# Optimization experiments

Hardware: AMD Instinct MI355X
Metric: run time of the kernel (lower is better)

Reference implementation:

```python
import jax, jax.numpy as jnp
import numpy as np

D_MODEL = 512
NUM_HEADS = 8
DFF = 2048
EPS = 1e-5


def _layernorm(x, gamma, beta):
    mu = jnp.mean(x, axis=-1, keepdims=True)
    var = jnp.mean(jnp.square(x - mu), axis=-1, keepdims=True)
    return (x - mu) / jnp.sqrt(var + EPS) * gamma + beta


def _mha(xq, xkv, wq, bq, wk, bk, wv, bv, wo, bo, mask):
    B, Sq, D = xq.shape
    Sk = xkv.shape[1]
    H = NUM_HEADS
    depth = D // H
    q = (xq @ wq + bq).reshape(B, Sq, H, depth).transpose(0, 2, 1, 3)  # bhqd
    k = (xkv @ wk + bk).reshape(B, Sk, H, depth).transpose(0, 2, 1, 3)  # bhkd
    v = (xkv @ wv + bv).reshape(B, Sk, H, depth).transpose(0, 2, 1, 3)  # bhkd
    logits = jnp.einsum('bhqd,bhkd->bhqk', q, k) / jnp.sqrt(jnp.float32(depth))
    if mask is not None:
        logits = logits + mask * -10000.0
    attn = jax.nn.softmax(logits, axis=-1)  # [B,H,Sq,Sk]
    out = jnp.einsum('bhqk,bhkd->bhqd', attn, v)
    out = out.transpose(0, 2, 1, 3).reshape(B, Sq, D)
    return out @ wo + bo, attn


def setup_inputs() -> dict:
    key = jax.random.key(0)
    ks = jax.random.split(key, 32)
    B, T, S, D, F = 8, 1024, 1024, D_MODEL, DFF
    sd = 1.0 / np.sqrt(D)
    inp = {
        'x': jax.random.normal(ks[0], (B, T, D), jnp.float32),
        'enc_output': jax.random.normal(ks[1], (B, S, D), jnp.float32),
        # causal mask: 1 where attention is disallowed (future positions)
        'look_ahead_mask': (1.0 - jnp.tril(jnp.ones((T, T), jnp.float32)))[None, None],
        'padding_mask': jnp.zeros((1, 1, 1, S), jnp.float32),
    }
    i = 2
    for pfx in ('1', '2'):
        for nm in ('wq', 'wk', 'wv', 'wo'):
            inp[nm + pfx] = jax.random.normal(ks[i], (D, D), jnp.float32) * sd; i += 1
            inp['b' + nm[1] + pfx if False else nm.replace('w', 'b') + pfx] = jnp.zeros((D,), jnp.float32)
    inp['w_ff1'] = jax.random.normal(ks[i], (D, F), jnp.float32) * sd; i += 1
    inp['b_ff1'] = jnp.zeros((F,), jnp.float32)
    inp['w_ff2'] = jax.random.normal(ks[i], (F, D), jnp.float32) / np.sqrt(F); i += 1
    inp['b_ff2'] = jnp.zeros((D,), jnp.float32)
    for j in ('1', '2', '3'):
        inp['gamma' + j] = jnp.ones((D,), jnp.float32)
        inp['beta' + j] = jnp.zeros((D,), jnp.float32)
    return inp


def reference(x, enc_output, look_ahead_mask, padding_mask,
              wq1, bq1, wk1, bk1, wv1, bv1, wo1, bo1,
              wq2, bq2, wk2, bk2, wv2, bv2, wo2, bo2,
              w_ff1, b_ff1, w_ff2, b_ff2,
              gamma1, beta1, gamma2, beta2, gamma3, beta3):
    # self-attention (dropout is identity: training=False)
    sa, sa_w = _mha(x, x, wq1, bq1, wk1, bk1, wv1, bv1, wo1, bo1, look_ahead_mask)
    out1 = _layernorm(x + sa, gamma1, beta1)
    # cross-attention
    ca, ca_w = _mha(out1, enc_output, wq2, bq2, wk2, bk2, wv2, bv2, wo2, bo2, padding_mask)
    out2 = _layernorm(out1 + ca, gamma2, beta2)
    # FFN
    ff = jax.nn.relu(out2 @ w_ff1 + b_ff1) @ w_ff2 + b_ff2
    out3 = _layernorm(out2 + ff, gamma3, beta3)
    return out3, sa_w, ca_w
```

## Files before the change

### kernel.cpp

```cpp
#include <hip/hip_runtime.h>
#include <hip/hip_bf16.h>


using bf16 = __hip_bfloat16;
typedef __attribute__((ext_vector_type(8))) short bf16x8v;
typedef __attribute__((ext_vector_type(4))) float f32x4;
typedef __attribute__((ext_vector_type(2))) float f32x2;
typedef __attribute__((ext_vector_type(2))) unsigned int u32x2;

#define DEVI __device__ __forceinline__

#define QSCL 0.18033688011112042f

DEVI short f2bs(float f) {
  bf16 h = __float2bfloat16(f);
  return *reinterpret_cast<short*>(&h);
}
DEVI bf16 f2b(float f) { return __float2bfloat16(f); }
DEVI float ex2(float x) { return __builtin_amdgcn_exp2f(x); }
DEVI float ldf(const float* p) { return *p; }
DEVI float ldf(const bf16* p) { return __bfloat162float(*p); }

DEVI void gload16(const bf16* g, bf16* l) {
  __builtin_amdgcn_global_load_lds(
      (const __attribute__((address_space(1))) void*)g,
      (__attribute__((address_space(3))) void*)l, 16, 0, 0);
}

DEVI void vmwait(int n) {
  if (n == 0)       asm volatile("s_waitcnt vmcnt(0)" ::: "memory");
  else if (n == 1)  asm volatile("s_waitcnt vmcnt(1)" ::: "memory");
  else if (n == 2)  asm volatile("s_waitcnt vmcnt(2)" ::: "memory");
  else if (n == 4)  asm volatile("s_waitcnt vmcnt(4)" ::: "memory");
  else if (n == 6)  asm volatile("s_waitcnt vmcnt(6)" ::: "memory");
  else if (n == 8)  asm volatile("s_waitcnt vmcnt(8)" ::: "memory");
  else              asm volatile("s_waitcnt vmcnt(10)" ::: "memory");
}
#define SBAR() __builtin_amdgcn_sched_barrier(0)

struct WDesc { const float* src; bf16* dst; int K; int N; int toff; float scl; };
struct PrepPack {
  const float* x; const float* enc; bf16* xb; bf16* encb;
  WDesc d[10];
  const float* bsrc[6]; float bscl[6]; float* bdst;
};

__global__ __launch_bounds__(256) void prep_k(PrepPack p) {
  const int bid = blockIdx.x;
  if (bid < 8192) {
    const float* s = (bid < 4096) ? p.x : p.enc;
    bf16* d = (bid < 4096) ? p.xb : p.encb;
    long i = ((long)(bid & 4095) * 256 + threadIdx.x) * 4;
    f32x4 v = *reinterpret_cast<const f32x4*>(s + i);
    union { short sh[4]; long l; } u;
    u.sh[0] = f2bs(v[0]); u.sh[1] = f2bs(v[1]); u.sh[2] = f2bs(v[2]); u.sh[3] = f2bs(v[3]);
    *reinterpret_cast<long*>(d + i) = u.l;
    return;
  }
  if (bid < 12288) {
    const int t = bid - 8192;
    int wi = 0;
#pragma unroll
    for (int i = 1; i < 10; i++)
      if (t >= p.d[i].toff) wi = i;
    const WDesc d = p.d[wi];
    const int lt = t - d.toff;
    const int nx = d.N >> 5;
    const int n0 = (lt % nx) * 32, k0 = (lt / nx) * 32;
    __shared__ float tile[32][33];
    const int tx = threadIdx.x & 31, ty = threadIdx.x >> 5;
#pragma unroll
    for (int i = 0; i < 32; i += 8)
      tile[ty + i][tx] = d.src[(long)(k0 + ty + i) * d.N + n0 + tx] * d.scl;
    __syncthreads();
#pragma unroll
    for (int i = 0; i < 32; i += 8)
      d.dst[(long)(n0 + ty + i) * d.K + k0 + tx] = f2b(tile[tx][ty + i]);
    return;
  }
  const int i = bid - 12288;
  const int e = threadIdx.x * 2;
  f32x2 v = *reinterpret_cast<const f32x2*>(p.bsrc[i] + e);
  v[0] *= p.bscl[i]; v[1] *= p.bscl[i];
  *reinterpret_cast<f32x2*>(p.bdst + i * 512 + e) = v;
}

template <int FM, int FN, typename TC, bool RELU, bool VTOUT>
DEVI void gemm_body(int bid, int nblocks,
                    const bf16* __restrict__ A, int lda,
                    const bf16* __restrict__ Bt, int ldb,
                    TC* __restrict__ C, int ldc,
                    const float* __restrict__ bias, int K, int tiles_n,
                    bf16* sA, bf16* sB,
                    bf16* __restrict__ vtout, int vcol0) {
  constexpr int BM = 32 * FM, BN = 32 * FN;
  const int tm8 = (nblocks / tiles_n) >> 3;
  const int r8 = bid >> 3;
  const int tm = (bid & 7) + ((r8 % tm8) << 3);
  const int tn = r8 / tm8;
  const int tid = threadIdx.x, wave = tid >> 6, lane = tid & 63;
  const int wr = wave >> 1, wc = wave & 1;
  const int l16 = lane & 15, lhi = lane >> 4;
  const int srow = lane >> 2, scol = (lane & 3) * 8;

  const bf16* Ab = A + (long)(tm * BM + wave * (BM / 4) + srow) * lda + scol;
  const bf16* Bb = Bt + (long)(tn * BN + wave * (BN / 4) + srow) * ldb + scol;

  auto stage = [&](int buf, int k0) {
#pragma unroll
    for (int i = 0; i < BM / 64; i++)
      gload16(Ab + (long)(i * 16) * lda + k0, sA + buf * BM * 32 + (wave * (BM / 4) + i * 16) * 32);
#pragma unroll
    for (int i = 0; i < BN / 64; i++)
      gload16(Bb + (long)(i * 16) * ldb + k0, sB + buf * BN * 32 + (wave * (BN / 4) + i * 16) * 32);
  };

  stage(0, 0);
  __syncthreads();

  f32x4 acc[FM][FN] = {};
  int cur = 0;
  for (int k0 = 0; k0 < K; k0 += 32) {
    if (k0 + 32 < K) stage(cur ^ 1, k0 + 32);
    bf16x8v af[FM], bfr[FN];
#pragma unroll
    for (int m = 0; m < FM; m++)
      af[m] = *reinterpret_cast<const bf16x8v*>(
          sA + cur * BM * 32 + (wr * 16 * FM + m * 16 + l16) * 32 + lhi * 8);
#pragma unroll
    for (int n = 0; n < FN; n++)
      bfr[n] = *reinterpret_cast<const bf16x8v*>(
          sB + cur * BN * 32 + (wc * 16 * FN + n * 16 + l16) * 32 + lhi * 8);
#pragma unroll
    for (int m = 0; m < FM; m++)
#pragma unroll
      for (int n = 0; n < FN; n++)
        acc[m][n] = __builtin_amdgcn_mfma_f32_16x16x32_bf16(af[m], bfr[n], acc[m][n], 0, 0, 0);
    if (k0 + 32 < K) {
      __syncthreads();
      cur ^= 1;
    }
  }

#pragma unroll
  for (int m = 0; m < FM; m++) {
    const int gr0 = tm * BM + wr * 16 * FM + m * 16 + lhi * 4;
#pragma unroll
    for (int n = 0; n < FN; n++) {
      const int gc = tn * BN + wc * 16 * FN + n * 16 + l16;
      const float bv = bias ? bias[gc] : 0.f;
      if (VTOUT && gc >= vcol0) {
        const int vc = gc - vcol0;
        bf16* vdst = vtout + ((long)(((gr0 >> 10) << 3) + (vc >> 6)) << 16)
                           + ((long)(vc & 63) << 10) + (gr0 & 1023);
        union { short sh[4]; u32x2 u2; } pk;
#pragma unroll
        for (int j = 0; j < 4; j++) pk.sh[j] = f2bs(acc[m][n][j] + bv);
        *reinterpret_cast<u32x2*>(vdst) = pk.u2;
      } else {
#pragma unroll
        for (int j = 0; j < 4; j++) {
          float v = acc[m][n][j] + bv;
          if (RELU) v = fmaxf(v, 0.f);
          if constexpr (sizeof(TC) == 4)
            C[(long)(gr0 + j) * ldc + gc] = v;
          else
            C[(long)(gr0 + j) * ldc + gc] = f2b(v);
        }
      }
    }
  }
}

template <int FM, int FN, typename TC, bool RELU>
__global__ __launch_bounds__(256) void gemm_gl_k(
    const bf16* __restrict__ A, int lda, const bf16* __restrict__ Bt, int ldb,
    TC* __restrict__ C, int ldc, const float* __restrict__ bias, int K, int tiles_n) {
  __shared__ bf16 sA[2 * 32 * FM * 32];
  __shared__ bf16 sB[2 * 32 * FN * 32];
  gemm_body<FM, FN, TC, RELU, false>(blockIdx.x, gridDim.x, A, lda, Bt, ldb, C, ldc,
                                     bias, K, tiles_n, sA, sB, nullptr, 0);
}

__global__ __launch_bounds__(256) void gemm_qkv_k(
    const bf16* __restrict__ A, const bf16* __restrict__ Bt, bf16* __restrict__ C,
    const float* __restrict__ bias, bf16* __restrict__ vt) {
  __shared__ bf16 sA[2 * 128 * 32];
  __shared__ bf16 sB[2 * 128 * 32];
  gemm_body<4, 4, bf16, false, true>(blockIdx.x, gridDim.x, A, 512, Bt, 512, C, 1536,
                                     bias, 512, 12, sA, sB, vt, 1024);
}

template <bool CAUSAL>
DEVI void attn_body(int bid, char* smem,
                    const bf16* __restrict__ Qm, int ldq,
                    const bf16* __restrict__ Km, int ldk,
                    const bf16* __restrict__ vt,
                    float* __restrict__ P, bf16* __restrict__ ctx) {
  bf16* Kst = (bf16*)smem;
  bf16* Vst = Kst + 3 * 2048;
  bf16* pst = Vst + 3 * 2048;
  const int bh = bid & 63;
  const int g = bid >> 6;
  const int qx = CAUSAL ? ((g < 4) ? g : 11 - g) : g;
  const int b = bh >> 3, h = bh & 7;
  const int tid = threadIdx.x, wave = tid >> 6, lane = tid & 63;
  const int l16 = lane & 15, lhi = lane >> 4;
  const int q0 = qx * 128 + wave * 32;
  const bf16* Qb = Qm + (long)(b * 1024 + q0) * ldq + h * 64;
  const bf16* Kb = Km + (long)b * 1024 * ldk + h * 64;
  const bf16* Vb = vt + (long)bh * 64 * 1024;

  const int nun = CAUSAL ? (q0 >> 5) : 32;
  const int nchw = CAUSAL ? nun + 1 : 32;
  const int nchb = CAUSAL ? qx * 4 + 4 : 32;

  const bf16* ksrc = Kb + (long)(tid >> 3) * ldk + ((tid & 7) ^ ((tid >> 3) & 7)) * 8;
  const bf16* vsrc = Vb + (long)(tid >> 2) * 1024 + ((tid & 3) ^ ((tid >> 2) & 3)) * 8;

  int kfo[2][2];
#pragma unroll
  for (int cc = 0; cc < 2; cc++) {
    const int r = cc * 16 + l16;
#pragma unroll
    for (int ks = 0; ks < 2; ks++)
      kfo[cc][ks] = r * 64 + (((ks * 64 + lhi * 16) ^ ((r & 7) << 4)) >> 1);
  }
  int vfo[4];
#pragma unroll
  for (int n = 0; n < 4; n++) {
    const int r = n * 16 + l16;
    vfo[n] = r * 32 + (((lhi * 16) ^ ((r & 3) << 4)) >> 1);
  }

  bf16x8v qB[2][2];
#pragma unroll
  for (int m = 0; m < 2; m++)
#pragma unroll
    for (int ks = 0; ks < 2; ks++)
      qB[m][ks] = *reinterpret_cast<const bf16x8v*>(
          Qb + (long)(m * 16 + l16) * ldq + ks * 32 + lhi * 8);

  float ll[2] = {0.f, 0.f};

  gload16(ksrc, Kst + wave * 512);
  gload16(ksrc + (long)32 * ldk, Kst + 2048 + wave * 512);
#pragma unroll 1
  for (int ch = 0; ch < nchb; ch++) {
    if (ch + 1 < nchb) vmwait(1); else vmwait(0);
    SBAR();
    __builtin_amdgcn_s_barrier();
    SBAR();
    if (ch + 2 < nchb)
      gload16(ksrc + (long)(ch + 2) * 32 * ldk, Kst + ((ch + 2) % 3) * 2048 + wave * 512);
    if (ch < nchw) {
      const int bo = (ch % 3) * 2048;
      bf16x8v kf[2][2];
#pragma unroll
      for (int cc = 0; cc < 2; cc++)
#pragma unroll
        for (int ks = 0; ks < 2; ks++)
          kf[cc][ks] = *reinterpret_cast<const bf16x8v*>(&Kst[bo + kfo[cc][ks]]);
      const bool diag = CAUSAL && (ch == nun);
#pragma unroll
      for (int m = 0; m < 2; m++) {
        f32x4 s0 = {}, s1 = {};
        s0 = __builtin_amdgcn_mfma_f32_16x16x32_bf16(kf[0][0], qB[m][0], s0, 0, 0, 0);
        s0 = __builtin_amdgcn_mfma_f32_16x16x32_bf16(kf[0][1], qB[m][1], s0, 0, 0, 0);
        s1 = __builtin_amdgcn_mfma_f32_16x16x32_bf16(kf[1][0], qB[m][0], s1, 0, 0, 0);
        s1 = __builtin_amdgcn_mfma_f32_16x16x32_bf16(kf[1][1], qB[m][1], s1, 0, 0, 0);
        if (diag) {
          const int rq = m * 16 + l16;
#pragma unroll
          for (int j = 0; j < 4; j++) {
            s0[j] = (lhi * 4 + j <= rq) ? s0[j] : -1e30f;
            s1[j] = (16 + lhi * 4 + j <= rq) ? s1[j] : -1e30f;
          }
        }
        float sum = 0.f;
#pragma unroll
        for (int j = 0; j < 4; j++) sum += ex2(s0[j]) + ex2(s1[j]);
        ll[m] += sum;
      }
    }
  }
  __syncthreads();

  float il[2];
#pragma unroll
  for (int m = 0; m < 2; m++) {
    float lo = ll[m];
    lo += __shfl_xor(lo, 16);
    lo += __shfl_xor(lo, 32);
    il[m] = 1.f / lo;
  }

  f32x4 pv[2][4] = {};
  float* Pg = P + (long)bh * 1024 * 1024 + (long)q0 * 1024;
  gload16(ksrc, Kst + wave * 512);
  gload16(vsrc, Vst + wave * 512);
  gload16(ksrc + (long)32 * ldk, Kst + 2048 + wave * 512);
  gload16(vsrc + 32, Vst + 2048 + wave * 512);
#pragma unroll 1
  for (int ch = 0; ch < nchb; ch++) {
    const int Sa = (ch >= 2 && ch - 2 < nchw) ? 4 : 0;
    const int Lr = (ch + 1 < nchb) ? 2 : 0;
    const int Sb = (ch >= 1 && ch - 1 < nchw) ? 4 : 0;
    vmwait(Sa + Lr + Sb);
    SBAR();
    __builtin_amdgcn_s_barrier();
    SBAR();
    if (ch + 2 < nchb) {
      gload16(ksrc + (long)(ch + 2) * 32 * ldk, Kst + ((ch + 2) % 3) * 2048 + wave * 512);
      gload16(vsrc + (ch + 2) * 32, Vst + ((ch + 2) % 3) * 2048 + wave * 512);
    }
    if (ch < nchw) {
      const int kc = ch * 32;
      const int bo = (ch % 3) * 2048;
      bf16x8v kf[2][2], vf[4];
#pragma unroll
      for (int cc = 0; cc < 2; cc++)
#pragma unroll
        for (int ks = 0; ks < 2; ks++)
          kf[cc][ks] = *reinterpret_cast<const bf16x8v*>(&Kst[bo + kfo[cc][ks]]);
#pragma unroll
      for (int n = 0; n < 4; n++)
        vf[n] = *reinterpret_cast<const bf16x8v*>(&Vst[bo + vfo[n]]);
      const bool diag = CAUSAL && (ch == nun);
#pragma unroll
      for (int m = 0; m < 2; m++) {
        f32x4 s0 = {}, s1 = {};
        s0 = __builtin_amdgcn_mfma_f32_16x16x32_bf16(kf[0][0], qB[m][0], s0, 0, 0, 0);
        s0 = __builtin_amdgcn_mfma_f32_16x16x32_bf16(kf[0][1], qB[m][1], s0, 0, 0, 0);
        s1 = __builtin_amdgcn_mfma_f32_16x16x32_bf16(kf[1][0], qB[m][0], s1, 0, 0, 0);
        s1 = __builtin_amdgcn_mfma_f32_16x16x32_bf16(kf[1][1], qB[m][1], s1, 0, 0, 0);
        if (diag) {
          const int rq = m * 16 + l16;
#pragma unroll
          for (int j = 0; j < 4; j++) {
            s0[j] = (lhi * 4 + j <= rq) ? s0[j] : -1e30f;
            s1[j] = (16 + lhi * 4 + j <= rq) ? s1[j] : -1e30f;
          }
        }
        f32x4 p0, p1;
#pragma unroll
        for (int j = 0; j < 4; j++) {
          p0[j] = ex2(s0[j]) * il[m];
          p1[j] = ex2(s1[j]) * il[m];
        }
        const int prow = (m * 16 + l16) * 40;
        union { short s[4]; u32x2 u; } pk0, pk1;
#pragma unroll
        for (int j = 0; j < 4; j++) { pk0.s[j] = f2bs(p0[j]); pk1.s[j] = f2bs(p1[j]); }
        *reinterpret_cast<u32x2*>(&pst[wave * 1280 + prow + lhi * 4]) = pk0.u;
        *reinterpret_cast<u32x2*>(&pst[wave * 1280 + prow + 16 + lhi * 4]) = pk1.u;
      }
#pragma unroll
      for (int m = 0; m < 2; m++) {
        bf16x8v pa = *reinterpret_cast<const bf16x8v*>(
            &pst[wave * 1280 + (m * 16 + l16) * 40 + lhi * 8]);
#pragma unroll
        for (int n = 0; n < 4; n++)
          pv[m][n] = __builtin_amdgcn_mfma_f32_16x16x32_bf16(pa, vf[n], pv[m][n], 0, 0, 0);
      }
#pragma unroll
      for (int f = 0; f < 4; f++) {
        const int row = f * 8 + (lane >> 3);
        u32x2 raw = *reinterpret_cast<const u32x2*>(
            &pst[wave * 1280 + row * 40 + (lane & 7) * 4]);
        union { unsigned int u; float fl; } c0, c1, c2, c3;
        c0.u = raw[0] << 16; c1.u = raw[0] & 0xffff0000u;
        c2.u = raw[1] << 16; c3.u = raw[1] & 0xffff0000u;
        f32x4 val = {c0.fl, c1.fl, c2.fl, c3.fl};
        __builtin_nontemporal_store(
            val, reinterpret_cast<f32x4*>(Pg + (long)row * 1024 + kc + (lane & 7) * 4));
      }
    }
  }

  bf16* cb = ctx + (long)(b * 1024 + q0) * 512 + h * 64;
#pragma unroll
  for (int m = 0; m < 2; m++)
#pragma unroll
    for (int n = 0; n < 4; n++)
#pragma unroll
      for (int j = 0; j < 4; j++)
        cb[(long)(m * 16 + lhi * 4 + j) * 512 + n * 16 + l16] = f2b(pv[m][n][j]);
}

template <bool CAUSAL>
__global__ __launch_bounds__(256) void attn_k(
    const bf16* __restrict__ Qm, int ldq, const bf16* __restrict__ Km, int ldk,
    const bf16* __restrict__ vt, float* __restrict__ P, bf16* __restrict__ ctx) {
  __shared__ __align__(16) char smem[34816];
  attn_body<CAUSAL>(blockIdx.x, smem, Qm, ldq, Km, ldk, vt, P, ctx);
}

__global__ __launch_bounds__(256) void attn_gemm_k(
    const bf16* __restrict__ Qm, int ldq, const bf16* __restrict__ Km, int ldk,
    const bf16* __restrict__ vt, float* __restrict__ P, bf16* __restrict__ ctx,
    const bf16* __restrict__ A, int lda, const bf16* __restrict__ Bt, int ldb,
    bf16* __restrict__ C, int ldc, const float* __restrict__ bias, int K, int tiles_n,
    bf16* __restrict__ vt2) {
  __shared__ __align__(16) char smem[34816];
  if (blockIdx.x < 512) {
    attn_body<true>(blockIdx.x, smem, Qm, ldq, Km, ldk, vt, P, ctx);
  } else {
    bf16* sA = (bf16*)smem;
    gemm_body<4, 4, bf16, false, true>(blockIdx.x - 512, 512, A, lda, Bt, ldb,
                                       C, ldc, bias, K, tiles_n, sA, sA + 8192,
                                       vt2, 512);
  }
}

template <typename TR>
__global__ __launch_bounds__(512) void gemm_ln_k(
    const bf16* __restrict__ A, int lda, const bf16* __restrict__ Bt,
    const float* __restrict__ bias, const TR* __restrict__ resid,
    const float* __restrict__ gamma, const float* __restrict__ beta,
    float* __restrict__ outf, bf16* __restrict__ outb, int K) {
  __shared__ bf16 sA[2][32 * 32];
  __shared__ bf16 sB[2][512 * 32];
  __shared__ float red[2][32][8];
  __shared__ f32x2 mr[32];
  const int tm = blockIdx.x;
  const int tid = threadIdx.x, wave = tid >> 6, lane = tid & 63;
  const int l16 = lane & 15, lhi = lane >> 4;

  const bf16* Asrc = A + (long)(tm * 32 + (tid >> 2)) * lda + (tid & 3) * 8;
  const bf16* Bsrc = Bt + (long)(tid >> 2) * K + (tid & 3) * 8;

  auto stage = [&](int buf, int k0) {
    if (tid < 128) gload16(Asrc + k0, &sA[buf][(tid >> 6) * 512]);
#pragma unroll
    for (int p = 0; p < 4; p++)
      gload16(Bsrc + (long)(p * 128) * K + k0, &sB[buf][p * 4096 + wave * 512]);
  };

  stage(0, 0);
  __syncthreads();

  f32x4 acc[2][4] = {};
  int cur = 0;
  for (int k0 = 0; k0 < K; k0 += 32) {
    if (k0 + 32 < K) stage(cur ^ 1, k0 + 32);
    bf16x8v af[2], bfr[4];
#pragma unroll
    for (int m = 0; m < 2; m++)
      af[m] = *reinterpret_cast<const bf16x8v*>(&sA[cur][(m * 16 + l16) * 32 + lhi * 8]);
#pragma unroll
    for (int n = 0; n < 4; n++)
      bfr[n] = *reinterpret_cast<const bf16x8v*>(&sB[cur][(wave * 64 + n * 16 + l16) * 32 + lhi * 8]);
#pragma unroll
    for (int m = 0; m < 2; m++)
#pragma unroll
      for (int n = 0; n < 4; n++)
        acc[m][n] = __builtin_amdgcn_mfma_f32_16x16x32_bf16(af[m], bfr[n], acc[m][n], 0, 0, 0);
    if (k0 + 32 < K) {
      __syncthreads();
      cur ^= 1;
    }
  }

  float bv[4], gm[4], bt[4];
#pragma unroll
  for (int n = 0; n < 4; n++) {
    const int gc = wave * 64 + n * 16 + l16;
    bv[n] = bias[gc]; gm[n] = gamma[gc]; bt[n] = beta[gc];
  }
  float v[2][4][4], rs[2][4], rq[2][4];
#pragma unroll
  for (int m = 0; m < 2; m++)
#pragma unroll
    for (int j = 0; j < 4; j++) { rs[m][j] = 0.f; rq[m][j] = 0.f; }
#pragma unroll
  for (int m = 0; m < 2; m++) {
#pragma unroll
    for (int j = 0; j < 4; j++) {
      const long grow = tm * 32 + m * 16 + lhi * 4 + j;
#pragma unroll
      for (int n = 0; n < 4; n++) {
        const int gc = wave * 64 + n * 16 + l16;
        const float val = acc[m][n][j] + bv[n] + ldf(resid + grow * 512 + gc);
        v[m][n][j] = val;
        rs[m][j] += val;
        rq[m][j] += val * val;
      }
    }
  }
#pragma unroll
  for (int m = 0; m < 2; m++)
#pragma unroll
    for (int j = 0; j < 4; j++)
#pragma unroll
      for (int off = 1; off <= 8; off <<= 1) {
        rs[m][j] += __shfl_xor(rs[m][j], off);
        rq[m][j] += __shfl_xor(rq[m][j], off);
      }
  if (l16 == 0) {
#pragma unroll
    for (int m = 0; m < 2; m++)
#pragma unroll
      for (int j = 0; j < 4; j++) {
        red[0][m * 16 + lhi * 4 + j][wave] = rs[m][j];
        red[1][m * 16 + lhi * 4 + j][wave] = rq[m][j];
      }
  }
  __syncthreads();
  if (tid < 32) {
    float s = 0.f, q = 0.f;
#pragma unroll
    for (int w = 0; w < 8; w++) { s += red[0][tid][w]; q += red[1][tid][w]; }
    const float mean = s * (1.f / 512.f);
    const float var = q * (1.f / 512.f) - mean * mean;
    f32x2 o = {mean, rsqrtf(var + 1e-5f)};
    mr[tid] = o;
  }
  __syncthreads();
#pragma unroll
  for (int m = 0; m < 2; m++) {
#pragma unroll
    for (int j = 0; j < 4; j++) {
      const int row = m * 16 + lhi * 4 + j;
      const f32x2 mrv = mr[row];
      const long grow = tm * 32 + row;
#pragma unroll
      for (int n = 0; n < 4; n++) {
        const int gc = wave * 64 + n * 16 + l16;
        const float o = (v[m][n][j] - mrv[0]) * mrv[1] * gm[n] + bt[n];
        if (outf) outf[grow * 512 + gc] = o;
        if (outb) outb[grow * 512 + gc] = f2b(o);
      }
    }
  }
}

extern "C" void kernel_launch(void* const* d_in, const int* in_sizes, int n_in,
                              void* d_out, int out_size, void* d_ws, size_t ws_size,
                              hipStream_t stream) {
  const float* x = (const float*)d_in[0];
  const float* enc = (const float*)d_in[1];
  const float* wq1 = (const float*)d_in[4];  const float* bq1 = (const float*)d_in[5];
  const float* wk1 = (const float*)d_in[6];  const float* bk1 = (const float*)d_in[7];
  const float* wv1 = (const float*)d_in[8];  const float* bv1 = (const float*)d_in[9];
  const float* wo1 = (const float*)d_in[10]; const float* bo1 = (const float*)d_in[11];
  const float* wq2 = (const float*)d_in[12]; const float* bq2 = (const float*)d_in[13];
  const float* wk2 = (const float*)d_in[14]; const float* bk2 = (const float*)d_in[15];
  const float* wv2 = (const float*)d_in[16]; const float* bv2 = (const float*)d_in[17];
  const float* wo2 = (const float*)d_in[18]; const float* bo2 = (const float*)d_in[19];
  const float* wff1 = (const float*)d_in[20]; const float* bff1 = (const float*)d_in[21];
  const float* wff2 = (const float*)d_in[22]; const float* bff2 = (const float*)d_in[23];
  const float* gamma1 = (const float*)d_in[24]; const float* beta1 = (const float*)d_in[25];
  const float* gamma2 = (const float*)d_in[26]; const float* beta2 = (const float*)d_in[27];
  const float* gamma3 = (const float*)d_in[28]; const float* beta3 = (const float*)d_in[29];

  float* out3 = (float*)d_out;
  float* sa_w = out3 + (long)8 * 1024 * 512;
  float* ca_w = sa_w + (long)64 * 1024 * 1024;

  char* w = (char*)d_ws;
  auto alloc = [&](long bytes) { char* p = w; w += (bytes + 255) & ~255L; return p; };
  bf16* xb     = (bf16*)alloc(8192L * 512 * 2);
  bf16* encb   = (bf16*)alloc(8192L * 512 * 2);
  bf16* wqkv1t = (bf16*)alloc(1536L * 512 * 2);
  bf16* wo1t   = (bf16*)alloc(512L * 512 * 2);
  bf16* wq2t   = (bf16*)alloc(512L * 512 * 2);
  bf16* wkv2t  = (bf16*)alloc(1024L * 512 * 2);
  bf16* wo2t   = (bf16*)alloc(512L * 512 * 2);
  bf16* wff1t  = (bf16*)alloc(2048L * 512 * 2);
  bf16* wff2t  = (bf16*)alloc(512L * 2048 * 2);
  float* bcat  = (float*)alloc(3072L * 4);
  bf16* qkv    = (bf16*)alloc(8192L * 1536 * 2);
  bf16* q2b    = (bf16*)alloc(8192L * 512 * 2);
  bf16* kv2    = (bf16*)alloc(8192L * 1024 * 2);
  bf16* vt     = (bf16*)alloc(64L * 64 * 1024 * 2);
  bf16* vt2    = (bf16*)alloc(64L * 64 * 1024 * 2);
  bf16* ctx    = (bf16*)alloc(8192L * 512 * 2);
  bf16* out1b  = (bf16*)alloc(8192L * 512 * 2);
  bf16* out2b  = (bf16*)alloc(8192L * 512 * 2);
  bf16* ffh    = qkv;

  PrepPack pp;
  pp.x = x; pp.enc = enc; pp.xb = xb; pp.encb = encb;
  pp.d[0] = {wq1,  wqkv1t,               512,  512,  0,    QSCL};
  pp.d[1] = {wk1,  wqkv1t + 512L * 512,  512,  512,  256,  1.f};
  pp.d[2] = {wv1,  wqkv1t + 1024L * 512, 512,  512,  512,  1.f};
  pp.d[3] = {wo1,  wo1t,                 512,  512,  768,  1.f};
  pp.d[4] = {wq2,  wq2t,                 512,  512,  1024, QSCL};
  pp.d[5] = {wk2,  wkv2t,                512,  512,  1280, 1.f};
  pp.d[6] = {wv2,  wkv2t + 512L * 512,   512,  512,  1536, 1.f};
  pp.d[7] = {wo2,  wo2t,                 512,  512,  1792, 1.f};
  pp.d[8] = {wff1, wff1t,                512,  2048, 2048, 1.f};
  pp.d[9] = {wff2, wff2t,                2048, 512,  3072, 1.f};
  pp.bsrc[0] = bq1; pp.bsrc[1] = bk1; pp.bsrc[2] = bv1;
  pp.bsrc[3] = bk2; pp.bsrc[4] = bv2; pp.bsrc[5] = bq2;
  pp.bscl[0] = QSCL; pp.bscl[1] = 1.f; pp.bscl[2] = 1.f;
  pp.bscl[3] = 1.f;  pp.bscl[4] = 1.f; pp.bscl[5] = QSCL;
  pp.bdst = bcat;
  prep_k<<<12294, 256, 0, stream>>>(pp);

  gemm_qkv_k<<<768, 256, 0, stream>>>(xb, wqkv1t, qkv, bcat, vt);
  attn_gemm_k<<<1024, 256, 0, stream>>>(
      qkv, 1536, qkv + 512, 1536, vt, sa_w, ctx,
      encb, 512, wkv2t, 512, kv2, 1024, bcat + 1536, 512, 8, vt2);
  gemm_ln_k<float><<<256, 512, 0, stream>>>(
      ctx, 512, wo1t, bo1, x, gamma1, beta1, nullptr, out1b, 512);

  gemm_gl_k<2, 4, bf16, false><<<512, 256, 0, stream>>>(
      out1b, 512, wq2t, 512, q2b, 512, bcat + 2560, 512, 4);
  attn_k<false><<<512, 256, 0, stream>>>(
      q2b, 512, kv2, 1024, vt2, ca_w, ctx);
  gemm_ln_k<bf16><<<256, 512, 0, stream>>>(
      ctx, 512, wo2t, bo2, out1b, gamma2, beta2, nullptr, out2b, 512);

  gemm_gl_k<4, 4, bf16, true><<<1024, 256, 0, stream>>>(
      out2b, 512, wff1t, 512, ffh, 2048, bff1, 512, 16);
  gemm_ln_k<bf16><<<256, 512, 0, stream>>>(
      ffh, 2048, wff2t, bff2, out2b, gamma3, beta3, out3, nullptr, 2048);
}
```

Measured before the change: 370.3 us.

## Replace QKV and FFN1 GEMMs with 256x256-tile 8-wave GEMM kernel

Adds a new GEMM kernel using 256x256 output tiles, a K-step of 64, 512 threads (8 waves, each computing 128x64), XOR-swizzled LDS and double-buffered global-to-LDS loads. The self-attention QKV projection and the FFN1 projection now use it in place of the 128x128-tile kernels. Larger tiles raise arithmetic intensity and cut global and LDS traffic per FLOP. In exchange the grids shrink to 192 and 256 blocks, so GPU occupancy and wave-level parallelism are lower, and register pressure is higher.

```diff
diff --git a/kernel.cpp b/kernel.cpp
--- a/kernel.cpp
+++ b/kernel.cpp
@@ -182,13 +182,109 @@
                                      bias, K, tiles_n, sA, sB, nullptr, 0);
 }
 
-__global__ __launch_bounds__(256) void gemm_qkv_k(
-    const bf16* __restrict__ A, const bf16* __restrict__ Bt, bf16* __restrict__ C,
-    const float* __restrict__ bias, bf16* __restrict__ vt) {
-  __shared__ bf16 sA[2 * 128 * 32];
-  __shared__ bf16 sB[2 * 128 * 32];
-  gemm_body<4, 4, bf16, false, true>(blockIdx.x, gridDim.x, A, 512, Bt, 512, C, 1536,
-                                     bias, 512, 12, sA, sB, vt, 1024);
+template <bool RELU, bool VTOUT>
+__global__ __launch_bounds__(512, 2) void gemm8_k(
+    const bf16* __restrict__ A, int lda, const bf16* __restrict__ Bt, int ldb,
+    bf16* __restrict__ C, int ldc, const float* __restrict__ bias, int K, int tiles_n,
+    bf16* __restrict__ vtout, int vcol0) {
+  __shared__ bf16 sA[2][256 * 64];
+  __shared__ bf16 sB[2][256 * 64];
+  const int NKT = K >> 6;
+  const int bid = blockIdx.x;
+  const int tm8 = ((int)gridDim.x / tiles_n) >> 3;
+  const int r8 = bid >> 3;
+  const int tm = (bid & 7) + ((r8 % tm8) << 3);
+  const int tn = r8 / tm8;
+  const int tid = threadIdx.x, wave = tid >> 6, lane = tid & 63;
+  const int wm = wave >> 2, wn = wave & 3;
+  const int l16 = lane & 15, lhi = lane >> 4;
+
+  const int srow = tid >> 3;
+  const int scol = ((tid & 7) ^ (srow & 7)) * 8;
+  const bf16* Ag = A + (long)(tm * 256 + srow) * lda + scol;
+  const bf16* Bg = Bt + (long)(tn * 256 + srow) * ldb + scol;
+
+  auto stage = [&](int buf, int kt) {
+    const int kofs = kt * 64;
+#pragma unroll
+    for (int p = 0; p < 4; p++)
+      gload16(Ag + (long)(p * 64) * lda + kofs, &sA[buf][(p * 64 + wave * 8) * 64]);
+#pragma unroll
+    for (int p = 0; p < 4; p++)
+      gload16(Bg + (long)(p * 64) * ldb + kofs, &sB[buf][(p * 64 + wave * 8) * 64]);
+  };
+
+  stage(0, 0);
+  if (NKT > 1) stage(1, 1);
+
+  f32x4 acc[8][4] = {};
+  const int sxor = (l16 & 7) << 4;
+  const int aoff0 = ((lhi * 16) ^ sxor) >> 1;
+  const int aoff1 = ((64 + lhi * 16) ^ sxor) >> 1;
+
+#pragma unroll 1
+  for (int kt = 0; kt < NKT; kt++) {
+    const int buf = kt & 1;
+    vmwait((kt + 1 < NKT) ? 8 : 0);
+    SBAR();
+    __builtin_amdgcn_s_barrier();
+    SBAR();
+#pragma unroll
+    for (int ks = 0; ks < 2; ks++) {
+      const int ao = ks ? aoff1 : aoff0;
+      bf16x8v bfr[4];
+#pragma unroll
+      for (int n = 0; n < 4; n++)
+        bfr[n] = *reinterpret_cast<const bf16x8v*>(
+            &sB[buf][(wn * 64 + n * 16 + l16) * 64 + ao]);
+#pragma unroll
+      for (int mh = 0; mh < 2; mh++) {
+        bf16x8v af[4];
+#pragma unroll
+        for (int mm = 0; mm < 4; mm++)
+          af[mm] = *reinterpret_cast<const bf16x8v*>(
+              &sA[buf][(wm * 128 + (mh * 4 + mm) * 16 + l16) * 64 + ao]);
+        __builtin_amdgcn_s_setprio(1);
+#pragma unroll
+        for (int mm = 0; mm < 4; mm++)
+#pragma unroll
+          for (int n = 0; n < 4; n++)
+            acc[mh * 4 + mm][n] = __builtin_amdgcn_mfma_f32_16x16x32_bf16(
+                af[mm], bfr[n], acc[mh * 4 + mm][n], 0, 0, 0);
+        __builtin_amdgcn_s_setprio(0);
+      }
+    }
+    SBAR();
+    __builtin_amdgcn_s_barrier();
+    SBAR();
+    if (kt + 2 < NKT) stage(buf, kt + 2);
+  }
+
+#pragma unroll
+  for (int m = 0; m < 8; m++) {
+    const int gr0 = tm * 256 + wm * 128 + m * 16 + lhi * 4;
+#pragma unroll
+    for (int n = 0; n < 4; n++) {
+      const int gc = tn * 256 + wn * 64 + n * 16 + l16;
+      const float bv = bias[gc];
+      if (VTOUT && gc >= vcol0) {
+        const int vc = gc - vcol0;
+        bf16* vdst = vtout + ((long)(((gr0 >> 10) << 3) + (vc >> 6)) << 16)
+                           + ((long)(vc & 63) << 10) + (gr0 & 1023);
+        union { short sh[4]; u32x2 u2; } pk;
+#pragma unroll
+        for (int j = 0; j < 4; j++) pk.sh[j] = f2bs(acc[m][n][j] + bv);
+        *reinterpret_cast<u32x2*>(vdst) = pk.u2;
+      } else {
+#pragma unroll
+        for (int j = 0; j < 4; j++) {
+          float v = acc[m][n][j] + bv;
+          if (RELU) v = fmaxf(v, 0.f);
+          C[(long)(gr0 + j) * ldc + gc] = f2b(v);
+        }
+      }
+    }
+  }
 }
 
 template <bool CAUSAL>
@@ -599,7 +695,8 @@
   pp.bdst = bcat;
   prep_k<<<12294, 256, 0, stream>>>(pp);
 
-  gemm_qkv_k<<<768, 256, 0, stream>>>(xb, wqkv1t, qkv, bcat, vt);
+  gemm8_k<false, true><<<192, 512, 0, stream>>>(
+      xb, 512, wqkv1t, 512, qkv, 1536, bcat, 512, 6, vt, 1024);
   attn_gemm_k<<<1024, 256, 0, stream>>>(
       qkv, 1536, qkv + 512, 1536, vt, sa_w, ctx,
       encb, 512, wkv2t, 512, kv2, 1024, bcat + 1536, 512, 8, vt2);
@@ -613,8 +710,8 @@
   gemm_ln_k<bf16><<<256, 512, 0, stream>>>(
       ctx, 512, wo2t, bo2, out1b, gamma2, beta2, nullptr, out2b, 512);
 
-  gemm_gl_k<4, 4, bf16, true><<<1024, 256, 0, stream>>>(
-      out2b, 512, wff1t, 512, ffh, 2048, bff1, 512, 16);
+  gemm8_k<true, false><<<256, 512, 0, stream>>>(
+      out2b, 512, wff1t, 512, ffh, 2048, bff1, 512, 8, nullptr, 0);
   gemm_ln_k<bf16><<<256, 512, 0, stream>>>(
       ffh, 2048, wff2t, bff2, out2b, gamma3, beta3, out3, nullptr, 2048);
 }
```

Result: faster. 355.3 us (-4.0%).
